# Optimization experiments

Measured on AMD Instinct MI355X. Metric: run time of the kernel, lower is better.

## Reference

```python
import jax, jax.numpy as jnp
import numpy as np

IN_SIZE = 1024
OUT_SIZE = 4096
LOGN = 12          # ceil(log2(max(in,out)))
N = 1 << LOGN      # 4096
BATCH = 8192


def setup_inputs() -> dict:
    key = jax.random.key(0)
    k1, k2, k3 = jax.random.split(key, 3)
    # kaiming_uniform on [2*logN, N]: fan_in = N, bound = sqrt(6/fan_in)
    bound = float(np.sqrt(6.0 / N))
    learned_params = jax.random.uniform(k1, (2 * LOGN, N), minval=-bound, maxval=bound, dtype=jnp.float32)
    inp = jax.random.normal(k2, (BATCH, IN_SIZE), dtype=jnp.float32)
    # np.random.permutation(N)[:out_size]
    out_row_indices = jax.random.permutation(k3, N)[:OUT_SIZE].astype(jnp.int32)
    return {"input": inp, "learned_params": learned_params, "out_row_indices": out_row_indices}


def reference(input, learned_params, out_row_indices):
    # Build B = prod_i (diag(p[2i]) + P_i @ diag(p[2i+1])), P_i[j, j^2^i] = 1.
    # (P_i @ diag(d) @ B)[j, :] = d[j^2^i] * B[j^2^i, :], so each layer is a
    # row-scale + xor-permuted row-scale of B (same math as the dense matmul chain).
    B = jnp.eye(N, dtype=input.dtype)
    for i in range(LOGN):
        perm = jnp.arange(N) ^ (1 << i)  # static per layer
        B = learned_params[2 * i][:, None] * B + learned_params[2 * i + 1][perm][:, None] * B[perm]
    layer_matrix = B[out_row_indices, :IN_SIZE]   # [out_size, in_size]
    return input @ layer_matrix.T                  # [batch, out_size]
```

## Files before the change

### kernel.cpp

```cpp
#include <hip/hip_runtime.h>


typedef float f4 __attribute__((ext_vector_type(4)));
typedef float f2 __attribute__((ext_vector_type(2)));
typedef int   i4 __attribute__((ext_vector_type(4)));

__device__ __forceinline__ int swz(int e) {
    return e ^ (((e >> 5) & 3) << 2);
}

template<int CTRL>
__device__ __forceinline__ float dppx(float x) {
    int xi = __builtin_bit_cast(int, x);
    int r  = __builtin_amdgcn_update_dpp(xi, xi, CTRL, 0xF, 0xF, true);
    return __builtin_bit_cast(float, r);
}

__global__ void __launch_bounds__(256) bfly_prep(
    const float* __restrict__ lp, const int* __restrict__ orow,
    float* __restrict__ scale, int* __restrict__ src2)
{
    int j = blockIdx.x * 256 + threadIdx.x;
    if (j >= 4096) return;
    int r = orow[j];
    int c = r & 1023;
    int u = r & 2047;
    const float* A10 = lp + 20 * 4096;
    const float* B10 = lp + 21 * 4096;
    const float* A11 = lp + 22 * 4096;
    const float* B11 = lp + 23 * 4096;
    float f11 = (r & 2048) ? B11[u] : A11[u];
    float f10 = (r & 1024) ? B10[c] : A10[c];
    scale[j] = f11 * f10;
    src2[j] = c ^ (((c >> 4) & 7) << 1);
}

__global__ void __launch_bounds__(512, 2) bfly_main(
    const float* __restrict__ inp, const float* __restrict__ lp,
    const float* __restrict__ scale, const int* __restrict__ src2,
    float* __restrict__ out)
{
    __shared__ __align__(16) float cf[20 * 1024 + 8 * 2048];
    const int t = threadIdx.x;
    const int wave = t >> 6, lane = t & 63;

    #pragma unroll
    for (int step = 0; step < 10; ++step) {
        const int q = 2 * step + (t >> 8);
        const int e = (t & 255) * 4;
        const f4 v = *reinterpret_cast<const f4*>(lp + (size_t)q * 4096 + e);
        *reinterpret_cast<f4*>(&cf[q * 1024 + swz(e)]) = v;
    }

    const int sBase = blockIdx.x * 16 + wave * 2;
    float x[2][16];
    #pragma unroll
    for (int m = 0; m < 2; ++m) {
        const f4* p = reinterpret_cast<const f4*>(inp + (size_t)(sBase + m) * 1024 + lane * 16);
        #pragma unroll
        for (int c = 0; c < 4; ++c) {
            f4 v = p[c];
            x[m][4*c+0] = v.x; x[m][4*c+1] = v.y; x[m][4*c+2] = v.z; x[m][4*c+3] = v.w;
        }
    }

    __syncthreads();

    #pragma unroll
    for (int i = 0; i < 2; ++i) {
        const float* arow = &cf[(size_t)(2*i)     * 1024];
        const float* brow = &cf[(size_t)(2*i + 1) * 1024];
        #pragma unroll
        for (int c = 0; c < 4; ++c) {
            f4 va = *reinterpret_cast<const f4*>(&arow[swz(lane * 16 + 4 * c)]);
            f4 vb = *reinterpret_cast<const f4*>(&brow[swz(lane * 16 + 4 * c)]);
            #pragma unroll
            for (int m = 0; m < 2; ++m) {
                float* xm = x[m];
                if (i == 0) {
                    float lo0 = xm[4*c+0], hi0 = xm[4*c+1];
                    xm[4*c+0] = va[0] * lo0 + vb[1] * hi0;
                    xm[4*c+1] = va[1] * hi0 + vb[0] * lo0;
                    float lo1 = xm[4*c+2], hi1 = xm[4*c+3];
                    xm[4*c+2] = va[2] * lo1 + vb[3] * hi1;
                    xm[4*c+3] = va[3] * hi1 + vb[2] * lo1;
                } else {
                    float lo0 = xm[4*c+0], hi0 = xm[4*c+2];
                    xm[4*c+0] = va[0] * lo0 + vb[2] * hi0;
                    xm[4*c+2] = va[2] * hi0 + vb[0] * lo0;
                    float lo1 = xm[4*c+1], hi1 = xm[4*c+3];
                    xm[4*c+1] = va[1] * lo1 + vb[3] * hi1;
                    xm[4*c+3] = va[3] * hi1 + vb[1] * lo1;
                }
            }
        }
    }

    #pragma unroll
    for (int i = 2; i < 4; ++i) {
        const float* arow = &cf[(size_t)(2*i)     * 1024];
        const float* brow = &cf[(size_t)(2*i + 1) * 1024];
        #pragma unroll
        for (int g = 0; g < 2; ++g) {
            const int q0 = (i == 2) ? 2 * g : g;
            const int q1 = (i == 2) ? q0 + 1 : q0 + 2;
            f4 va0 = *reinterpret_cast<const f4*>(&arow[swz(lane * 16 + 4 * q0)]);
            f4 va1 = *reinterpret_cast<const f4*>(&arow[swz(lane * 16 + 4 * q1)]);
            f4 vb0 = *reinterpret_cast<const f4*>(&brow[swz(lane * 16 + 4 * q0)]);
            f4 vb1 = *reinterpret_cast<const f4*>(&brow[swz(lane * 16 + 4 * q1)]);
            #pragma unroll
            for (int m = 0; m < 2; ++m) {
                float* xm = x[m];
                #pragma unroll
                for (int e = 0; e < 4; ++e) {
                    float lo = xm[4*q0+e], hi = xm[4*q1+e];
                    xm[4*q0+e] = va0[e] * lo + vb1[e] * hi;
                    xm[4*q1+e] = va1[e] * hi + vb0[e] * lo;
                }
            }
        }
    }

    {
        const float* arow = &cf[(size_t)8 * 1024];
        const float* brow = &cf[(size_t)9 * 1024];
        #pragma unroll
        for (int c = 0; c < 4; ++c) {
            f4 va = *reinterpret_cast<const f4*>(&arow[swz(lane * 16 + 4 * c)]);
            f4 vb = *reinterpret_cast<const f4*>(&brow[swz((lane ^ 1) * 16 + 4 * c)]);
            #pragma unroll
            for (int m = 0; m < 2; ++m) {
                #pragma unroll
                for (int e = 0; e < 4; ++e) {
                    float v = x[m][4*c+e];
                    x[m][4*c+e] = va[e] * v + vb[e] * dppx<0xB1>(v);
                }
            }
        }
    }

    #pragma unroll
    for (int i = 5; i < 10; ++i) {
        const int d = 1 << (i - 4);
        const float* arow = &cf[(size_t)(2*i)     * 1024];
        const float* brow = &cf[(size_t)(2*i + 1) * 1024];
        #pragma unroll
        for (int c = 0; c < 4; ++c) {
            f4 va = *reinterpret_cast<const f4*>(&arow[swz(lane * 16 + 4 * c)]);
            f4 vb = *reinterpret_cast<const f4*>(&brow[swz((lane ^ d) * 16 + 4 * c)]);
            #pragma unroll
            for (int m = 0; m < 2; ++m) {
                #pragma unroll
                for (int e = 0; e < 4; ++e) {
                    float v = x[m][4*c+e];
                    float xp = (d == 2) ? dppx<0x4E>(v)
                             : (d == 8) ? dppx<0x128>(v)
                             :            __shfl_xor(v, d, 64);
                    x[m][4*c+e] = va[e] * v + vb[e] * xp;
                }
            }
        }
    }

    float* zz = &cf[20 * 1024 + (size_t)wave * 2048];
    const int km0 = (lane & 7) << 1;
    #pragma unroll
    for (int k = 0; k < 16; k += 2) {
        int pi = lane * 16 + (k ^ km0);
        f4 v = { x[0][k], x[1][k], x[0][k+1], x[1][k+1] };
        *reinterpret_cast<f4*>(&zz[2 * pi]) = v;
    }

    const i4* srv = reinterpret_cast<const i4*>(src2);
    const f4* scv = reinterpret_cast<const f4*>(scale);
    f4* o0 = reinterpret_cast<f4*>(out + (size_t)sBase * 4096);
    f4* o1 = reinterpret_cast<f4*>(out + (size_t)(sBase + 1) * 4096);

    i4 si = srv[lane];
    f4 sc = scv[lane];
    #pragma unroll
    for (int it = 0; it < 16; ++it) {
        i4 si_c = si;
        f4 sc_c = sc;
        if (it + 1 < 16) {
            si = srv[(it + 1) * 64 + lane];
            sc = scv[(it + 1) * 64 + lane];
        }
        int j4 = it * 64 + lane;
        f2 vx = *reinterpret_cast<const f2*>(&zz[2 * si_c.x]);
        f2 vy = *reinterpret_cast<const f2*>(&zz[2 * si_c.y]);
        f2 vz = *reinterpret_cast<const f2*>(&zz[2 * si_c.z]);
        f2 vw = *reinterpret_cast<const f2*>(&zz[2 * si_c.w]);
        f4 r0 = { sc_c.x * vx.x, sc_c.y * vy.x, sc_c.z * vz.x, sc_c.w * vw.x };
        f4 r1 = { sc_c.x * vx.y, sc_c.y * vy.y, sc_c.z * vz.y, sc_c.w * vw.y };
        o0[j4] = r0;
        o1[j4] = r1;
    }
}

extern "C" void kernel_launch(void* const* d_in, const int* in_sizes, int n_in,
                              void* d_out, int out_size, void* d_ws, size_t ws_size,
                              hipStream_t stream) {
    const float* inp  = (const float*)d_in[0];
    const float* lp   = (const float*)d_in[1];
    const int*   orow = (const int*)d_in[2];
    float* out = (float*)d_out;

    float* scale = (float*)d_ws;
    int*   src2  = (int*)((char*)d_ws + 4096 * 4);

    bfly_prep<<<16, 256, 0, stream>>>(lp, orow, scale, src2);
    bfly_main<<<512, 512, 0, stream>>>(inp, lp, scale, src2, out);
}
```

Measured before the change: 42.47 us.

## Process two sample pairs per wave, prefetching second input during first emit

Each block now handles 32 samples (4 per wave) and the grid is halved, so the per-block LDS load of the butterfly coefficients is amortised over twice the work. The second pair's input is loaded before the first pair's output gather/store, overlapping global loads with the output phase. The per-wave zz staging buffer is reused between the two passes. In exchange, register pressure rises, fewer blocks fill the GPU's CUs, and the grid becomes a single partial wave.

Measured after the change: 139.9 us. +229.3%, slower.

```diff
diff --git a/kernel.cpp b/kernel.cpp
--- a/kernel.cpp
+++ b/kernel.cpp
@@ -35,37 +35,23 @@
     src2[j] = c ^ (((c >> 4) & 7) << 1);
 }
 
-__global__ void __launch_bounds__(512, 2) bfly_main(
-    const float* __restrict__ inp, const float* __restrict__ lp,
-    const float* __restrict__ scale, const int* __restrict__ src2,
-    float* __restrict__ out)
-{
-    __shared__ __align__(16) float cf[20 * 1024 + 8 * 2048];
-    const int t = threadIdx.x;
-    const int wave = t >> 6, lane = t & 63;
-
-    #pragma unroll
-    for (int step = 0; step < 10; ++step) {
-        const int q = 2 * step + (t >> 8);
-        const int e = (t & 255) * 4;
-        const f4 v = *reinterpret_cast<const f4*>(lp + (size_t)q * 4096 + e);
-        *reinterpret_cast<f4*>(&cf[q * 1024 + swz(e)]) = v;
-    }
-
-    const int sBase = blockIdx.x * 16 + wave * 2;
-    float x[2][16];
+__device__ __forceinline__ void load_chunk(
+    const float* __restrict__ inp, int s0, int lane, float (&x)[2][16])
+{
     #pragma unroll
     for (int m = 0; m < 2; ++m) {
-        const f4* p = reinterpret_cast<const f4*>(inp + (size_t)(sBase + m) * 1024 + lane * 16);
+        const f4* p = reinterpret_cast<const f4*>(inp + (size_t)(s0 + m) * 1024 + lane * 16);
         #pragma unroll
         for (int c = 0; c < 4; ++c) {
             f4 v = p[c];
             x[m][4*c+0] = v.x; x[m][4*c+1] = v.y; x[m][4*c+2] = v.z; x[m][4*c+3] = v.w;
         }
     }
-
-    __syncthreads();
-
+}
+
+__device__ __forceinline__ void butterfly(
+    const float* __restrict__ cf, int lane, float (&x)[2][16])
+{
     #pragma unroll
     for (int i = 0; i < 2; ++i) {
         const float* arow = &cf[(size_t)(2*i)     * 1024];
@@ -161,8 +147,11 @@
             }
         }
     }
-
-    float* zz = &cf[20 * 1024 + (size_t)wave * 2048];
+}
+
+__device__ __forceinline__ void zwrite(
+    float* __restrict__ zz, int lane, const float (&x)[2][16])
+{
     const int km0 = (lane & 7) << 1;
     #pragma unroll
     for (int k = 0; k < 16; k += 2) {
@@ -170,11 +159,17 @@
         f4 v = { x[0][k], x[1][k], x[0][k+1], x[1][k+1] };
         *reinterpret_cast<f4*>(&zz[2 * pi]) = v;
     }
-
+}
+
+__device__ __forceinline__ void emit(
+    const float* __restrict__ zz, const int* __restrict__ src2,
+    const float* __restrict__ scale, float* __restrict__ out,
+    int s0, int lane)
+{
     const i4* srv = reinterpret_cast<const i4*>(src2);
     const f4* scv = reinterpret_cast<const f4*>(scale);
-    f4* o0 = reinterpret_cast<f4*>(out + (size_t)sBase * 4096);
-    f4* o1 = reinterpret_cast<f4*>(out + (size_t)(sBase + 1) * 4096);
+    f4* o0 = reinterpret_cast<f4*>(out + (size_t)s0 * 4096);
+    f4* o1 = reinterpret_cast<f4*>(out + (size_t)(s0 + 1) * 4096);
 
     i4 si = srv[lane];
     f4 sc = scv[lane];
@@ -198,6 +193,44 @@
     }
 }
 
+__global__ void __launch_bounds__(512, 2) bfly_main(
+    const float* __restrict__ inp, const float* __restrict__ lp,
+    const float* __restrict__ scale, const int* __restrict__ src2,
+    float* __restrict__ out)
+{
+    __shared__ __align__(16) float cf[20 * 1024 + 8 * 2048];
+    const int t = threadIdx.x;
+    const int wave = t >> 6, lane = t & 63;
+
+    #pragma unroll
+    for (int step = 0; step < 10; ++step) {
+        const int q = 2 * step + (t >> 8);
+        const int e = (t & 255) * 4;
+        const f4 v = *reinterpret_cast<const f4*>(lp + (size_t)q * 4096 + e);
+        *reinterpret_cast<f4*>(&cf[q * 1024 + swz(e)]) = v;
+    }
+
+    const int sBase = blockIdx.x * 32 + wave * 4;
+    float* zz = &cf[20 * 1024 + (size_t)wave * 2048];
+
+    float x[2][16];
+    load_chunk(inp, sBase, lane, x);
+
+    __syncthreads();
+
+    butterfly(cf, lane, x);
+    zwrite(zz, lane, x);
+
+    float y[2][16];
+    load_chunk(inp, sBase + 2, lane, y);
+
+    emit(zz, src2, scale, out, sBase, lane);
+
+    butterfly(cf, lane, y);
+    zwrite(zz, lane, y);
+    emit(zz, src2, scale, out, sBase + 2, lane);
+}
+
 extern "C" void kernel_launch(void* const* d_in, const int* in_sizes, int n_in,
                               void* d_out, int out_size, void* d_ws, size_t ws_size,
                               hipStream_t stream) {
@@ -210,5 +243,5 @@
     int*   src2  = (int*)((char*)d_ws + 4096 * 4);
 
     bfly_prep<<<16, 256, 0, stream>>>(lp, orow, scale, src2);
-    bfly_main<<<512, 512, 0, stream>>>(inp, lp, scale, src2, out);
-}
+    bfly_main<<<256, 512, 0, stream>>>(inp, lp, scale, src2, out);
+}
```
